# Performance work log

Measured on AMD Instinct MI355X. Metric: run time of the kernel, lower is better.

The kernel has to match this reference:

```python
import jax, jax.numpy as jnp
import numpy as np

B, D, H, W, C = 2, 16, 56, 56, 128
WD, WH, WW = 2, 7, 7
SD, SH, SW = 1, 3, 3
HEADS = 4
HEAD_DIM = C // HEADS
N = WD * WH * WW            # tokens per window = 98
NW = (D // WD) * (H // WH) * (W // WW)  # windows per batch = 512
EPS = 1e-5
SCALE = HEAD_DIM ** -0.5


def _partition_np(x):
    b, d, h, w, c = x.shape
    x = x.reshape(b, d // WD, WD, h // WH, WH, w // WW, WW, c)
    return x.transpose(0, 1, 3, 5, 2, 4, 6, 7).reshape(-1, N, c)


def _compute_attn_mask():
    # cyclic-shift mask: label 3x3x3 regions, windows mix labels -> -100
    img = np.zeros((1, D, H, W, 1), np.float32)
    cnt = 0
    for ds in (slice(0, -WD), slice(-WD, -SD), slice(-SD, None)):
        for hs in (slice(0, -WH), slice(-WH, -SH), slice(-SH, None)):
            for ws in (slice(0, -WW), slice(-WW, -SW), slice(-SW, None)):
                img[:, ds, hs, ws, :] = cnt
                cnt += 1
    mw = _partition_np(img).reshape(-1, N)          # (nW, N)
    am = mw[:, None, :] - mw[:, :, None]
    return np.where(am != 0, -100.0, 0.0).astype(np.float32)


def _rel_index():
    coords = np.stack(np.meshgrid(np.arange(WD), np.arange(WH), np.arange(WW), indexing='ij')).reshape(3, -1)
    rel = (coords[:, :, None] - coords[:, None, :]).transpose(1, 2, 0)  # (N,N,3)
    rel[..., 0] += WD - 1
    rel[..., 1] += WH - 1
    rel[..., 2] += WW - 1
    rel[..., 0] *= (2 * WH - 1) * (2 * WW - 1)
    rel[..., 1] *= 2 * WW - 1
    return rel.sum(-1).astype(np.int32)  # (N,N)


def setup_inputs() -> dict:
    key = jax.random.key(0)
    ks = jax.random.split(key, 8)
    s = 0.02
    table_size = (2 * WD - 1) * (2 * WH - 1) * (2 * WW - 1)
    return {
        'x': jax.random.normal(ks[0], (B, D, H, W, C), jnp.float32),
        'attn_mask': jnp.asarray(_compute_attn_mask()),
        'rel_index': jnp.asarray(_rel_index()),
        'norm1_g': jnp.ones((C,), jnp.float32),
        'norm1_b': jnp.zeros((C,), jnp.float32),
        'qkv_w': jax.random.normal(ks[1], (C, 3 * C), jnp.float32) * s,
        'qkv_b': jnp.zeros((3 * C,), jnp.float32),
        'rel_table': jax.random.normal(ks[2], (table_size, HEADS), jnp.float32) * s,
        'proj_w': jax.random.normal(ks[3], (C, C), jnp.float32) * s,
        'proj_b': jnp.zeros((C,), jnp.float32),
        'norm2_g': jnp.ones((C,), jnp.float32),
        'norm2_b': jnp.zeros((C,), jnp.float32),
        'fc1_w': jax.random.normal(ks[4], (C, 4 * C), jnp.float32) * s,
        'fc1_b': jnp.zeros((4 * C,), jnp.float32),
        'fc2_w': jax.random.normal(ks[5], (4 * C, C), jnp.float32) * s,
        'fc2_b': jnp.zeros((C,), jnp.float32),
    }


def _ln(x, g, b):
    mu = jnp.mean(x, -1, keepdims=True)
    var = jnp.mean(jnp.square(x - mu), -1, keepdims=True)
    return (x - mu) * jax.lax.rsqrt(var + EPS) * g + b


def _block(x, attn_mask, rel_index, norm1_g, norm1_b, qkv_w, qkv_b, rel_table,
           proj_w, proj_b, norm2_g, norm2_b, fc1_w, fc1_b, fc2_w, fc2_b):
    # ---- part1: LN -> shift -> window partition -> W-MSA -> reverse -> unshift
    h = _ln(x, norm1_g, norm1_b)
    h = jnp.roll(h, (-SD, -SH, -SW), axis=(1, 2, 3))
    # window partition -> (B*nW, N, C)
    h = h.reshape(B, D // WD, WD, H // WH, WH, W // WW, WW, C)
    h = h.transpose(0, 1, 3, 5, 2, 4, 6, 7).reshape(B * NW, N, C)
    qkv = (h @ qkv_w + qkv_b).reshape(B * NW, N, 3, HEADS, HEAD_DIM)
    qkv = qkv.transpose(2, 0, 3, 1, 4)  # (3, B_, heads, N, hd)
    q, k, v = qkv[0] * SCALE, qkv[1], qkv[2]
    attn = jnp.einsum('bhnd,bhmd->bhnm', q, k)  # (B_, heads, N, N)
    bias = rel_table[rel_index.reshape(-1)].reshape(N, N, HEADS).transpose(2, 0, 1)
    attn = attn + bias[None]
    attn = attn.reshape(B, NW, HEADS, N, N) + attn_mask[None, :, None]
    attn = jax.nn.softmax(attn.reshape(B * NW, HEADS, N, N), axis=-1)
    o = jnp.einsum('bhnm,bhmd->bhnd', attn, v)
    o = o.transpose(0, 2, 1, 3).reshape(B * NW, N, C)
    o = o @ proj_w + proj_b
    # window reverse -> (B, D, H, W, C)
    o = o.reshape(B, D // WD, H // WH, W // WW, WD, WH, WW, C)
    o = o.transpose(0, 1, 4, 2, 5, 3, 6, 7).reshape(B, D, H, W, C)
    o = jnp.roll(o, (SD, SH, SW), axis=(1, 2, 3))
    x = x + o  # drop_path = identity (rate 0)
    # ---- part2: LN -> MLP (keras gelu is exact, approximate=False)
    m = _ln(x, norm2_g, norm2_b)
    m = jax.nn.gelu(m @ fc1_w + fc1_b, approximate=False) @ fc2_w + fc2_b
    return x + m


def reference(x, attn_mask, rel_index, norm1_g, norm1_b, qkv_w, qkv_b, rel_table,
              proj_w, proj_b, norm2_g, norm2_b, fc1_w, fc1_b, fc2_w, fc2_b):
    return _block(x, attn_mask, rel_index, norm1_g, norm1_b, qkv_w, qkv_b, rel_table,
                  proj_w, proj_b, norm2_g, norm2_b, fc1_w, fc1_b, fc2_w, fc2_b)
```

## Files before the change

### kernel.cpp

```cpp
#include <hip/hip_runtime.h>
#include <math.h>

#define ROWS 100352
#define EPSL 1e-5f
#define SCALE_Q 0.17677669529663687f

typedef __attribute__((ext_vector_type(8))) short bf16x8;
typedef __attribute__((ext_vector_type(4))) float f32x4;

__device__ __forceinline__ unsigned short f2b(float f) {
  union { float f; unsigned int u; } a; a.f = f;
  unsigned int u = a.u;
  return (unsigned short)((u + 0x7FFF + ((u >> 16) & 1)) >> 16);
}

__device__ __forceinline__ int map_row(int r) {
  int t = r;
  int tw = t % 7; t /= 7;
  int th = t % 7; t /= 7;
  int td = t & 1;  t >>= 1;
  int zw = t & 7;  t >>= 3;
  int zh = t & 7;  t >>= 3;
  int zd = t & 7;  int bb = t >> 3;
  int d = zd * 2 + td;
  int h = zh * 7 + th;
  int w = zw * 7 + tw;
  int sd = (d + 1) & 15;
  int sh = h + 3; if (sh >= 56) sh -= 56;
  int sw = w + 3; if (sw >= 56) sw -= 56;
  return ((bb * 16 + sd) * 56 + sh) * 56 + sw;
}

__global__ __launch_bounds__(256) void k_prep_all(
    const float* __restrict__ qkv_w, unsigned short* __restrict__ qkvT,
    const float* __restrict__ proj_w, unsigned short* __restrict__ projT,
    const float* __restrict__ fc1_w, unsigned short* __restrict__ fc1T,
    const float* __restrict__ fc2_w, unsigned short* __restrict__ fc2T)
{
  int b = blockIdx.x, tid = threadIdx.x;
  if (b < 192) {
    int id = b * 256 + tid;
    int n = id >> 7, k = id & 127;
    float v = qkv_w[(size_t)k * 384 + n];
    if (n < 128) v *= SCALE_Q;
    qkvT[id] = f2b(v);
  } else if (b < 256) {
    int id = (b - 192) * 256 + tid;
    int n = id >> 7, k = id & 127;
    projT[id] = f2b(proj_w[(size_t)k * 128 + n]);
  } else if (b < 512) {
    int id = (b - 256) * 256 + tid;
    int n = id >> 7, k = id & 127;
    fc1T[id] = f2b(fc1_w[(size_t)k * 512 + n]);
  } else {
    int id = (b - 512) * 256 + tid;
    int n = id >> 9, k = id & 511;
    fc2T[id] = f2b(fc2_w[(size_t)k * 128 + n]);
  }
}

__global__ __launch_bounds__(256) void k_prep_biasC(
    const int* __restrict__ relidx, const float* __restrict__ rtab,
    float* __restrict__ biasC)
{
  int id = blockIdx.x * 256 + threadIdx.x;
  int l  = id & 63;  int t = id >> 6;
  int ct = t % 7;    t /= 7;
  int rt = t & 7;    t >>= 3;
  int h  = t & 3;    int wm = t >> 2;
  int n0 = rt*16 + ((l >> 4) << 2);
  int m  = ct*16 + (l & 15);
  float4 v;
  float* vp = &v.x;
  int cm = 0;
  if (m < 98)
    cm = (m >= 49 ? 1 : 0) | ((m % 49) >= 28 ? 2 : 0) | ((m % 7) >= 4 ? 4 : 0);
  #pragma unroll
  for (int r = 0; r < 4; ++r) {
    int n = n0 + r;
    float val;
    if (m >= 98) val = -10000.f;
    else if (n >= 98) val = 0.f;
    else {
      val = rtab[relidx[n*98 + m]*4 + h];
      int cn = (n >= 49 ? 1 : 0) | ((n % 49) >= 28 ? 2 : 0) | ((n % 7) >= 4 ? 4 : 0);
      if ((cn ^ cm) & wm) val -= 100.f;
    }
    vp[r] = val;
  }
  *(float4*)(biasC + (size_t)id*4) = v;
}

__global__ __launch_bounds__(256) void k_qkv(
    const float* __restrict__ x, const float* __restrict__ g,
    const float* __restrict__ bta, const unsigned short* __restrict__ Wt,
    const float* __restrict__ bias, unsigned short* __restrict__ out)
{
  __shared__ unsigned short As[128 * 136];
  int tid = threadIdx.x;
  int row0 = blockIdx.x * 128;
  {
    int grp = tid >> 5, lane = tid & 31;
    float4 gv = *(const float4*)(g + lane*4);
    float4 bv = *(const float4*)(bta + lane*4);
    #pragma unroll
    for (int p = 0; p < 16; ++p) {
      int r = p * 8 + grp;
      size_t src = (size_t)map_row(row0 + r);
      float4 v = *(const float4*)(x + src * 128 + lane * 4);
      float s  = v.x + v.y + v.z + v.w;
      float ss = v.x*v.x + v.y*v.y + v.z*v.z + v.w*v.w;
      #pragma unroll
      for (int o = 16; o; o >>= 1) {
        s  += __shfl_xor(s,  o, 32);
        ss += __shfl_xor(ss, o, 32);
      }
      float mu   = s * (1.f/128.f);
      float rstd = rsqrtf(ss * (1.f/128.f) - mu*mu + EPSL);
      ushort4 o4;
      o4.x = f2b((v.x-mu)*rstd*gv.x + bv.x);
      o4.y = f2b((v.y-mu)*rstd*gv.y + bv.y);
      o4.z = f2b((v.z-mu)*rstd*gv.z + bv.z);
      o4.w = f2b((v.w-mu)*rstd*gv.w + bv.w);
      *(ushort4*)&As[r*136 + lane*4] = o4;
    }
  }
  __syncthreads();
  int l = tid & 63, w = tid >> 6;
  int wr = (w >> 1) * 64, wc = (w & 1) * 64;
  int fr = l & 15, gq = l >> 4, fk = gq * 8;
  for (int c = 0; c < 3; ++c) {
    int col0 = c * 128;
    float bmul = (c == 0) ? SCALE_Q : 1.f;
    f32x4 acc[4][4] = {};
    #pragma unroll
    for (int ks = 0; ks < 128; ks += 32) {
      bf16x8 af[4], bv[4];
      #pragma unroll
      for (int n = 0; n < 4; ++n)
        bv[n] = *(const bf16x8*)(Wt + (size_t)(col0 + wc + n*16 + fr)*128 + ks + fk);
      #pragma unroll
      for (int m = 0; m < 4; ++m)
        af[m] = *(bf16x8*)&As[(wr + m*16 + fr)*136 + ks + fk];
      #pragma unroll
      for (int m = 0; m < 4; ++m)
        #pragma unroll
        for (int n = 0; n < 4; ++n)
          acc[m][n] = __builtin_amdgcn_mfma_f32_16x16x32_bf16(af[m], bv[n], acc[m][n], 0, 0, 0);
    }
    #pragma unroll
    for (int m = 0; m < 4; ++m)
      #pragma unroll
      for (int r = 0; r < 4; ++r) {
        int grow = row0 + wr + m*16 + gq*4 + r;
        #pragma unroll
        for (int n = 0; n < 4; ++n) {
          int col = col0 + wc + n*16 + fr;
          out[(size_t)grow*384 + col] = f2b(acc[m][n][r] + bias[col]*bmul);
        }
      }
  }
}

__global__ __launch_bounds__(256, 4) void k_attn_mfma(
    const unsigned short* __restrict__ qkv,
    const float* __restrict__ biasC,
    unsigned short* __restrict__ o_part)
{
  __shared__ unsigned short Vt[32 * 136];
  __shared__ unsigned short Pb[128 * 120];
  int tid  = threadIdx.x;
  int head = blockIdx.x & 3;
  int win  = blockIdx.x >> 2;
  int widx = win & 511;
  int wm = ((widx >> 6) == 7 ? 1 : 0) | (((widx >> 3) & 7) == 7 ? 2 : 0)
         | ((widx & 7) == 7 ? 4 : 0);
  const unsigned short* base = qkv + (size_t)win * 98 * 384 + head * 32;

  for (int it = tid; it < 32 * 128; it += 256) {
    int d = it & 31, m = it >> 5;
    unsigned short v = 0;
    if (m < 98) v = base[m*384 + 256 + d];
    Vt[d*136 + m] = v;
  }
  for (int it = tid; it < 128 * 8; it += 256) {
    int n = it >> 3, c2 = 112 + (it & 7);
    Pb[n*120 + c2] = 0;
  }

  int l = tid & 63, w = tid >> 6;
  int fr = l & 15, g = l >> 4, fk = g * 8;
  bf16x8 zero8 = {0,0,0,0,0,0,0,0};

  bf16x8 aq[2];
  #pragma unroll
  for (int lt = 0; lt < 2; ++lt) {
    int row = (w*2 + lt)*16 + fr;
    aq[lt] = (row < 98) ? *(const bf16x8*)(base + row*384 + fk) : zero8;
  }

  const float* bcb = biasC + (size_t)(wm*4 + head) * 8 * 7 * 256;
  f32x4 S[2][7];
  #pragma unroll
  for (int ct = 0; ct < 7; ++ct) {
    int m = ct*16 + fr;
    bf16x8 kb = (m < 98) ? *(const bf16x8*)(base + m*384 + 128 + fk) : zero8;
    #pragma unroll
    for (int lt = 0; lt < 2; ++lt) {
      f32x4 bc = *(const f32x4*)(bcb + ((w*2 + lt)*7 + ct)*256 + l*4);
      S[lt][ct] = __builtin_amdgcn_mfma_f32_16x16x32_bf16(aq[lt], kb, bc, 0, 0, 0);
    }
  }

  #pragma unroll
  for (int lt = 0; lt < 2; ++lt) {
    #pragma unroll
    for (int r = 0; r < 4; ++r) {
      float mx = S[lt][0][r];
      #pragma unroll
      for (int ct = 1; ct < 7; ++ct) mx = fmaxf(mx, S[lt][ct][r]);
      #pragma unroll
      for (int o = 8; o; o >>= 1) mx = fmaxf(mx, __shfl_xor(mx, o));
      float e[7], sum = 0.f;
      #pragma unroll
      for (int ct = 0; ct < 7; ++ct) { e[ct] = __expf(S[lt][ct][r] - mx); sum += e[ct]; }
      #pragma unroll
      for (int o = 8; o; o >>= 1) sum += __shfl_xor(sum, o);
      float inv = 1.f / sum;
      #pragma unroll
      for (int ct = 0; ct < 7; ++ct) S[lt][ct][r] = e[ct] * inv;
    }
  }

  #pragma unroll
  for (int lt = 0; lt < 2; ++lt)
    #pragma unroll
    for (int ct = 0; ct < 7; ++ct) {
      int m = ct*16 + fr;
      #pragma unroll
      for (int r = 0; r < 4; ++r) {
        int n = w*32 + lt*16 + g*4 + r;
        Pb[n*120 + m] = f2b(S[lt][ct][r]);
      }
    }
  __syncthreads();

  f32x4 O[2][2] = {};
  #pragma unroll
  for (int ks = 0; ks < 4; ++ks) {
    bf16x8 ap[2], bv[2];
    #pragma unroll
    for (int lt = 0; lt < 2; ++lt) {
      int rowoff = ((w*2 + lt)*16 + fr)*120;
      if (ks < 3) ap[lt] = *(bf16x8*)&Pb[rowoff + ks*32 + fk];
      else        ap[lt] = (g < 2) ? *(bf16x8*)&Pb[rowoff + 96 + fk] : zero8;
    }
    #pragma unroll
    for (int vt = 0; vt < 2; ++vt)
      bv[vt] = *(bf16x8*)&Vt[(vt*16 + fr)*136 + ks*32 + fk];
    #pragma unroll
    for (int lt = 0; lt < 2; ++lt)
      #pragma unroll
      for (int vt = 0; vt < 2; ++vt)
        O[lt][vt] = __builtin_amdgcn_mfma_f32_16x16x32_bf16(ap[lt], bv[vt], O[lt][vt], 0, 0, 0);
  }

  #pragma unroll
  for (int lt = 0; lt < 2; ++lt)
    #pragma unroll
    for (int r = 0; r < 4; ++r) {
      int n = w*32 + lt*16 + g*4 + r;
      if (n < 98) {
        unsigned short* orow = o_part + ((size_t)win*98 + n)*128 + head*32;
        #pragma unroll
        for (int vt = 0; vt < 2; ++vt)
          orow[vt*16 + fr] = f2b(O[lt][vt][r]);
      }
    }
}

__global__ __launch_bounds__(256) void k_proj(
    const unsigned short* __restrict__ A,
    const unsigned short* __restrict__ Wt,
    const float* __restrict__ bias,
    const float* __restrict__ Xres, float* __restrict__ Cf)
{
  __shared__ unsigned short As[128 * 136];
  int tid = threadIdx.x;
  int row0 = blockIdx.x * 128;
  #pragma unroll
  for (int i = 0; i < 8; ++i) {
    int chunk = i * 256 + tid;
    int rr = chunk >> 4, off = (chunk & 15) * 8;
    *(uint4*)&As[rr*136 + off] = *(const uint4*)(A + (size_t)(row0+rr)*128 + off);
  }
  __syncthreads();
  int l = tid & 63, w = tid >> 6;
  int wr = (w >> 1) * 64, wc = (w & 1) * 64;
  int fr = l & 15, gq = l >> 4, fk = gq * 8;
  f32x4 acc[4][4] = {};
  #pragma unroll
  for (int ks = 0; ks < 128; ks += 32) {
    bf16x8 af[4], bv[4];
    #pragma unroll
    for (int n = 0; n < 4; ++n)
      bv[n] = *(const bf16x8*)(Wt + (size_t)(wc + n*16 + fr)*128 + ks + fk);
    #pragma unroll
    for (int m = 0; m < 4; ++m)
      af[m] = *(bf16x8*)&As[(wr + m*16 + fr)*136 + ks + fk];
    #pragma unroll
    for (int m = 0; m < 4; ++m)
      #pragma unroll
      for (int n = 0; n < 4; ++n)
        acc[m][n] = __builtin_amdgcn_mfma_f32_16x16x32_bf16(af[m], bv[n], acc[m][n], 0, 0, 0);
  }
  #pragma unroll
  for (int m = 0; m < 4; ++m)
    #pragma unroll
    for (int r = 0; r < 4; ++r) {
      int grow = row0 + wr + m*16 + gq*4 + r;
      size_t dst = (size_t)map_row(grow);
      #pragma unroll
      for (int n = 0; n < 4; ++n) {
        int col = wc + n*16 + fr;
        Cf[dst*128 + col] = acc[m][n][r] + bias[col] + Xres[dst*128 + col];
      }
    }
}

__global__ __launch_bounds__(512, 4) void k_mlp(
    float* __restrict__ xio,
    const float* __restrict__ g, const float* __restrict__ bta,
    const unsigned short* __restrict__ W1t,
    const float* __restrict__ b1,
    const unsigned short* __restrict__ W2t,
    const float* __restrict__ b2)
{
  __shared__ unsigned short As[128 * 136];
  __shared__ unsigned short Pb[128 * 136];
  int tid = threadIdx.x;
  int row0 = blockIdx.x * 128;
  {
    int grp = tid >> 5, lane = tid & 31;
    float4 gv = *(const float4*)(g + lane*4);
    float4 bv = *(const float4*)(bta + lane*4);
    #pragma unroll
    for (int p = 0; p < 8; ++p) {
      int r = p * 16 + grp;
      float4 v = *(const float4*)(xio + (size_t)(row0 + r) * 128 + lane * 4);
      float s  = v.x + v.y + v.z + v.w;
      float ss = v.x*v.x + v.y*v.y + v.z*v.z + v.w*v.w;
      #pragma unroll
      for (int o = 16; o; o >>= 1) {
        s  += __shfl_xor(s,  o, 32);
        ss += __shfl_xor(ss, o, 32);
      }
      float mu   = s * (1.f/128.f);
      float rstd = rsqrtf(ss * (1.f/128.f) - mu*mu + EPSL);
      ushort4 o4;
      o4.x = f2b((v.x-mu)*rstd*gv.x + bv.x);
      o4.y = f2b((v.y-mu)*rstd*gv.y + bv.y);
      o4.z = f2b((v.z-mu)*rstd*gv.z + bv.z);
      o4.w = f2b((v.w-mu)*rstd*gv.w + bv.w);
      *(ushort4*)&As[r*136 + lane*4] = o4;
    }
  }
  __syncthreads();
  int l = tid & 63, w = tid >> 6;
  int wr = (w & 1) * 64, wc = (w >> 1) * 32;
  int fr = l & 15, gq = l >> 4, fk = gq * 8;

  f32x4 O[4][2] = {};
  for (int j = 0; j < 4; ++j) {
    f32x4 S[4][2] = {};
    #pragma unroll
    for (int ks = 0; ks < 4; ++ks) {
      bf16x8 af[4], bv[2];
      #pragma unroll
      for (int n = 0; n < 2; ++n)
        bv[n] = *(const bf16x8*)(W1t + (size_t)(j*128 + wc + n*16 + fr)*128 + ks*32 + fk);
      #pragma unroll
      for (int m = 0; m < 4; ++m)
        af[m] = *(bf16x8*)&As[(wr + m*16 + fr)*136 + ks*32 + fk];
      #pragma unroll
      for (int m = 0; m < 4; ++m)
        #pragma unroll
        for (int n = 0; n < 2; ++n)
          S[m][n] = __builtin_amdgcn_mfma_f32_16x16x32_bf16(af[m], bv[n], S[m][n], 0, 0, 0);
    }
    #pragma unroll
    for (int m = 0; m < 4; ++m)
      #pragma unroll
      for (int n = 0; n < 2; ++n) {
        int col = wc + n*16 + fr;
        float bb = b1[j*128 + col];
        #pragma unroll
        for (int r = 0; r < 4; ++r) {
          float v = S[m][n][r] + bb;
          float u = 1.5957691216057308f * v * (1.f + 0.044715f*v*v);
          v = v / (1.f + __expf(-u));
          Pb[(wr + m*16 + gq*4 + r)*136 + col] = f2b(v);
        }
      }
    __syncthreads();
    #pragma unroll
    for (int ks = 0; ks < 4; ++ks) {
      bf16x8 ap[4], bv[2];
      #pragma unroll
      for (int n = 0; n < 2; ++n)
        bv[n] = *(const bf16x8*)(W2t + (size_t)(wc + n*16 + fr)*512 + j*128 + ks*32 + fk);
      #pragma unroll
      for (int m = 0; m < 4; ++m)
        ap[m] = *(bf16x8*)&Pb[(wr + m*16 + fr)*136 + ks*32 + fk];
      #pragma unroll
      for (int m = 0; m < 4; ++m)
        #pragma unroll
        for (int n = 0; n < 2; ++n)
          O[m][n] = __builtin_amdgcn_mfma_f32_16x16x32_bf16(ap[m], bv[n], O[m][n], 0, 0, 0);
    }
    __syncthreads();
  }
  #pragma unroll
  for (int m = 0; m < 4; ++m)
    #pragma unroll
    for (int r = 0; r < 4; ++r) {
      size_t grow = row0 + wr + m*16 + gq*4 + r;
      #pragma unroll
      for (int n = 0; n < 2; ++n) {
        int col = wc + n*16 + fr;
        xio[grow*128 + col] += O[m][n][r] + b2[col];
      }
    }
}

extern "C" void kernel_launch(void* const* d_in, const int* in_sizes, int n_in,
                              void* d_out, int out_size, void* d_ws, size_t ws_size,
                              hipStream_t stream)
{
  const float* x         = (const float*)d_in[0];
  const int*   rel_index = (const int*)  d_in[2];
  const float* n1g       = (const float*)d_in[3];
  const float* n1b       = (const float*)d_in[4];
  const float* qkv_w     = (const float*)d_in[5];
  const float* qkv_b     = (const float*)d_in[6];
  const float* rtab      = (const float*)d_in[7];
  const float* proj_w    = (const float*)d_in[8];
  const float* proj_b    = (const float*)d_in[9];
  const float* n2g       = (const float*)d_in[10];
  const float* n2b       = (const float*)d_in[11];
  const float* fc1_w     = (const float*)d_in[12];
  const float* fc1_b     = (const float*)d_in[13];
  const float* fc2_w     = (const float*)d_in[14];
  const float* fc2_b     = (const float*)d_in[15];
  float* out = (float*)d_out;

  unsigned short* buf0  = (unsigned short*)d_ws;
  unsigned short* buf1  = buf0 + (size_t)ROWS * 384;
  unsigned short* qkvT  = buf1 + (size_t)ROWS * 128;
  unsigned short* projT = qkvT + 384 * 128;
  unsigned short* fc1T  = projT + 128 * 128;
  unsigned short* fc2T  = fc1T + 512 * 128;
  float* biasC          = (float*)(fc2T + 128 * 512);

  k_prep_all<<<768, 256, 0, stream>>>(qkv_w, qkvT, proj_w, projT,
                                      fc1_w, fc1T, fc2_w, fc2T);
  k_prep_biasC<<<448, 256, 0, stream>>>(rel_index, rtab, biasC);

  k_qkv<<<ROWS/128, 256, 0, stream>>>(x, n1g, n1b, qkvT, qkv_b, buf0);

  k_attn_mfma<<<4096, 256, 0, stream>>>(buf0, biasC, buf1);

  k_proj<<<ROWS/128, 256, 0, stream>>>(buf1, projT, proj_b, x, out);

  k_mlp<<<ROWS/128, 512, 0, stream>>>(out, n2g, n2b, fc1T, fc1_b, fc2T, fc2_b);
}
```

Before: 238.1 us.

## Register-resident MLP: fold LN affine into fc1, drop LDS staging via bpermute

Rewrites the MLP kernel so each wave owns 32 tokens, keeps the normalized activations and the GELU hidden tile in registers, and uses the swapped-operand MFMA layout with ds_bpermute to reshape the hidden fragments instead of staging through shared memory with block barriers. The LayerNorm gamma is folded into the fc1 weights, and beta into a precomputed fc1 bias by a new small prep kernel. This removes LDS traffic and __syncthreads from the hot loop. In exchange each wave re-reads the weights from global/L2, register pressure rises (O[8][2] accumulators), and bf16 packing now uses the hardware cvt instruction.

```diff
diff --git a/kernel.cpp b/kernel.cpp
--- a/kernel.cpp
+++ b/kernel.cpp
@@ -12,6 +12,11 @@
   union { float f; unsigned int u; } a; a.f = f;
   unsigned int u = a.u;
   return (unsigned short)((u + 0x7FFF + ((u >> 16) & 1)) >> 16);
+}
+__device__ __forceinline__ unsigned cvtpk(float lo, float hi) {
+  unsigned r;
+  asm volatile("v_cvt_pk_bf16_f32 %0, %1, %2" : "=v"(r) : "v"(lo), "v"(hi));
+  return r;
 }
 
 __device__ __forceinline__ int map_row(int r) {
@@ -35,7 +40,8 @@
     const float* __restrict__ qkv_w, unsigned short* __restrict__ qkvT,
     const float* __restrict__ proj_w, unsigned short* __restrict__ projT,
     const float* __restrict__ fc1_w, unsigned short* __restrict__ fc1T,
-    const float* __restrict__ fc2_w, unsigned short* __restrict__ fc2T)
+    const float* __restrict__ fc2_w, unsigned short* __restrict__ fc2T,
+    const float* __restrict__ n2g)
 {
   int b = blockIdx.x, tid = threadIdx.x;
   if (b < 192) {
@@ -51,12 +57,23 @@
   } else if (b < 512) {
     int id = (b - 256) * 256 + tid;
     int n = id >> 7, k = id & 127;
-    fc1T[id] = f2b(fc1_w[(size_t)k * 512 + n]);
+    fc1T[id] = f2b(fc1_w[(size_t)k * 512 + n] * n2g[k]);
   } else {
     int id = (b - 512) * 256 + tid;
     int n = id >> 9, k = id & 511;
     fc2T[id] = f2b(fc2_w[(size_t)k * 128 + n]);
   }
+}
+
+__global__ __launch_bounds__(256) void k_prep_b1(
+    const float* __restrict__ fc1_b, const float* __restrict__ n2b,
+    const float* __restrict__ fc1_w, float* __restrict__ b1p)
+{
+  int h = blockIdx.x * 256 + threadIdx.x;
+  if (h >= 512) return;
+  float acc = fc1_b[h];
+  for (int k = 0; k < 128; ++k) acc += n2b[k] * fc1_w[(size_t)k * 512 + h];
+  b1p[h] = acc;
 }
 
 __global__ __launch_bounds__(256) void k_prep_biasC(
@@ -328,109 +345,132 @@
     }
 }
 
-__global__ __launch_bounds__(512, 4) void k_mlp(
+__global__ __launch_bounds__(256, 3) void k_mlp(
     float* __restrict__ xio,
-    const float* __restrict__ g, const float* __restrict__ bta,
     const unsigned short* __restrict__ W1t,
-    const float* __restrict__ b1,
+    const float* __restrict__ b1p,
     const unsigned short* __restrict__ W2t,
     const float* __restrict__ b2)
 {
-  __shared__ unsigned short As[128 * 136];
-  __shared__ unsigned short Pb[128 * 136];
   int tid = threadIdx.x;
-  int row0 = blockIdx.x * 128;
-  {
-    int grp = tid >> 5, lane = tid & 31;
-    float4 gv = *(const float4*)(g + lane*4);
-    float4 bv = *(const float4*)(bta + lane*4);
-    #pragma unroll
-    for (int p = 0; p < 8; ++p) {
-      int r = p * 16 + grp;
-      float4 v = *(const float4*)(xio + (size_t)(row0 + r) * 128 + lane * 4);
-      float s  = v.x + v.y + v.z + v.w;
-      float ss = v.x*v.x + v.y*v.y + v.z*v.z + v.w*v.w;
-      #pragma unroll
-      for (int o = 16; o; o >>= 1) {
-        s  += __shfl_xor(s,  o, 32);
-        ss += __shfl_xor(ss, o, 32);
-      }
-      float mu   = s * (1.f/128.f);
-      float rstd = rsqrtf(ss * (1.f/128.f) - mu*mu + EPSL);
-      ushort4 o4;
-      o4.x = f2b((v.x-mu)*rstd*gv.x + bv.x);
-      o4.y = f2b((v.y-mu)*rstd*gv.y + bv.y);
-      o4.z = f2b((v.z-mu)*rstd*gv.z + bv.z);
-      o4.w = f2b((v.w-mu)*rstd*gv.w + bv.w);
-      *(ushort4*)&As[r*136 + lane*4] = o4;
-    }
-  }
-  __syncthreads();
   int l = tid & 63, w = tid >> 6;
-  int wr = (w & 1) * 64, wc = (w >> 1) * 32;
-  int fr = l & 15, gq = l >> 4, fk = gq * 8;
-
-  f32x4 O[4][2] = {};
-  for (int j = 0; j < 4; ++j) {
-    f32x4 S[4][2] = {};
+  int i = l & 15, gl = l >> 4;
+  int fk = gl * 8;
+  int tok0 = blockIdx.x * 128 + w * 32;
+
+  int idx0 = (((l >> 4) & 1) * 32 + i) * 4;
+  int idx1 = idx0 + 64;
+  bool hiHalf = (l >= 32);
+
+  bf16x8 atok[2][4];
+  #pragma unroll
+  for (int t = 0; t < 2; ++t) {
+    const float* row = xio + (size_t)(tok0 + t*16 + i) * 128;
+    float v[4][8];
+    float s = 0.f, ss = 0.f;
     #pragma unroll
     for (int ks = 0; ks < 4; ++ks) {
-      bf16x8 af[4], bv[2];
-      #pragma unroll
-      for (int n = 0; n < 2; ++n)
-        bv[n] = *(const bf16x8*)(W1t + (size_t)(j*128 + wc + n*16 + fr)*128 + ks*32 + fk);
-      #pragma unroll
-      for (int m = 0; m < 4; ++m)
-        af[m] = *(bf16x8*)&As[(wr + m*16 + fr)*136 + ks*32 + fk];
-      #pragma unroll
-      for (int m = 0; m < 4; ++m)
+      float4 v0 = *(const float4*)(row + ks*32 + fk);
+      float4 v1 = *(const float4*)(row + ks*32 + fk + 4);
+      v[ks][0]=v0.x; v[ks][1]=v0.y; v[ks][2]=v0.z; v[ks][3]=v0.w;
+      v[ks][4]=v1.x; v[ks][5]=v1.y; v[ks][6]=v1.z; v[ks][7]=v1.w;
+      s += v0.x+v0.y+v0.z+v0.w + v1.x+v1.y+v1.z+v1.w;
+      ss += v0.x*v0.x+v0.y*v0.y+v0.z*v0.z+v0.w*v0.w
+          + v1.x*v1.x+v1.y*v1.y+v1.z*v1.z+v1.w*v1.w;
+    }
+    s  += __shfl_xor(s, 16);  s  += __shfl_xor(s, 32);
+    ss += __shfl_xor(ss, 16); ss += __shfl_xor(ss, 32);
+    float mu = s * (1.f/128.f);
+    float rstd = rsqrtf(ss * (1.f/128.f) - mu*mu + EPSL);
+    #pragma unroll
+    for (int ks = 0; ks < 4; ++ks) {
+      union { unsigned u[4]; bf16x8 v8; } pk;
+      #pragma unroll
+      for (int p = 0; p < 4; ++p)
+        pk.u[p] = cvtpk((v[ks][2*p]-mu)*rstd, (v[ks][2*p+1]-mu)*rstd);
+      atok[t][ks] = pk.v8;
+    }
+  }
+
+  f32x4 O[8][2] = {};
+  for (int j = 0; j < 16; ++j) {
+    f32x4 S[2][2] = {{{0.f,0.f,0.f,0.f},{0.f,0.f,0.f,0.f}},
+                     {{0.f,0.f,0.f,0.f},{0.f,0.f,0.f,0.f}}};
+    #pragma unroll
+    for (int ks = 0; ks < 4; ++ks) {
+      bf16x8 w1f[2];
+      #pragma unroll
+      for (int T = 0; T < 2; ++T)
+        w1f[T] = *(const bf16x8*)(W1t + (size_t)(j*32 + T*16 + i)*128 + ks*32 + fk);
+      #pragma unroll
+      for (int T = 0; T < 2; ++T)
         #pragma unroll
-        for (int n = 0; n < 2; ++n)
-          S[m][n] = __builtin_amdgcn_mfma_f32_16x16x32_bf16(af[m], bv[n], S[m][n], 0, 0, 0);
-    }
-    #pragma unroll
-    for (int m = 0; m < 4; ++m)
-      #pragma unroll
-      for (int n = 0; n < 2; ++n) {
-        int col = wc + n*16 + fr;
-        float bb = b1[j*128 + col];
+        for (int t = 0; t < 2; ++t)
+          S[T][t] = __builtin_amdgcn_mfma_f32_16x16x32_bf16(w1f[T], atok[t][ks], S[T][t], 0, 0, 0);
+    }
+    float b1v[2][4];
+    #pragma unroll
+    for (int T = 0; T < 2; ++T)
+      #pragma unroll
+      for (int r = 0; r < 4; ++r)
+        b1v[T][r] = b1p[j*32 + T*16 + gl*4 + r];
+    #pragma unroll
+    for (int T = 0; T < 2; ++T)
+      #pragma unroll
+      for (int t = 0; t < 2; ++t)
         #pragma unroll
         for (int r = 0; r < 4; ++r) {
-          float v = S[m][n][r] + bb;
-          float u = 1.5957691216057308f * v * (1.f + 0.044715f*v*v);
-          v = v / (1.f + __expf(-u));
-          Pb[(wr + m*16 + gq*4 + r)*136 + col] = f2b(v);
+          float vv = S[T][t][r] + b1v[T][r];
+          float u = 1.5957691216057308f * vv * (1.f + 0.044715f*vv*vv);
+          S[T][t][r] = vv / (1.f + __expf(-u));
         }
-      }
-    __syncthreads();
-    #pragma unroll
-    for (int ks = 0; ks < 4; ++ks) {
-      bf16x8 ap[4], bv[2];
-      #pragma unroll
-      for (int n = 0; n < 2; ++n)
-        bv[n] = *(const bf16x8*)(W2t + (size_t)(wc + n*16 + fr)*512 + j*128 + ks*32 + fk);
-      #pragma unroll
-      for (int m = 0; m < 4; ++m)
-        ap[m] = *(bf16x8*)&Pb[(wr + m*16 + fr)*136 + ks*32 + fk];
-      #pragma unroll
-      for (int m = 0; m < 4; ++m)
-        #pragma unroll
-        for (int n = 0; n < 2; ++n)
-          O[m][n] = __builtin_amdgcn_mfma_f32_16x16x32_bf16(ap[m], bv[n], O[m][n], 0, 0, 0);
-    }
-    __syncthreads();
-  }
-  #pragma unroll
-  for (int m = 0; m < 4; ++m)
-    #pragma unroll
-    for (int r = 0; r < 4; ++r) {
-      size_t grow = row0 + wr + m*16 + gq*4 + r;
-      #pragma unroll
-      for (int n = 0; n < 2; ++n) {
-        int col = wc + n*16 + fr;
-        xio[grow*128 + col] += O[m][n][r] + b2[col];
-      }
-    }
+    bf16x8 pf[2];
+    #pragma unroll
+    for (int t = 0; t < 2; ++t) {
+      int A = (int)cvtpk(S[0][t][0], S[0][t][1]);
+      int B = (int)cvtpk(S[0][t][2], S[0][t][3]);
+      int C = (int)cvtpk(S[1][t][0], S[1][t][1]);
+      int D = (int)cvtpk(S[1][t][2], S[1][t][3]);
+      union { unsigned u[4]; bf16x8 v8; } pk;
+      int a0 = __builtin_amdgcn_ds_bpermute(idx0, A);
+      int c0 = __builtin_amdgcn_ds_bpermute(idx0, C);
+      int b0 = __builtin_amdgcn_ds_bpermute(idx0, B);
+      int d0 = __builtin_amdgcn_ds_bpermute(idx0, D);
+      int a1 = __builtin_amdgcn_ds_bpermute(idx1, A);
+      int c1 = __builtin_amdgcn_ds_bpermute(idx1, C);
+      int b1r = __builtin_amdgcn_ds_bpermute(idx1, B);
+      int d1 = __builtin_amdgcn_ds_bpermute(idx1, D);
+      pk.u[0] = (unsigned)(hiHalf ? c0 : a0);
+      pk.u[1] = (unsigned)(hiHalf ? d0 : b0);
+      pk.u[2] = (unsigned)(hiHalf ? c1 : a1);
+      pk.u[3] = (unsigned)(hiHalf ? d1 : b1r);
+      pf[t] = pk.v8;
+    }
+    #pragma unroll
+    for (int jt = 0; jt < 8; ++jt) {
+      bf16x8 w2f = *(const bf16x8*)(W2t + (size_t)(jt*16 + i)*512 + j*32 + fk);
+      #pragma unroll
+      for (int t = 0; t < 2; ++t)
+        O[jt][t] = __builtin_amdgcn_mfma_f32_16x16x32_bf16(w2f, pf[t], O[jt][t], 0, 0, 0);
+    }
+  }
+
+  #pragma unroll
+  for (int t = 0; t < 2; ++t) {
+    float* row = xio + (size_t)(tok0 + t*16 + i) * 128;
+    #pragma unroll
+    for (int jt = 0; jt < 8; ++jt) {
+      int col = jt*16 + gl*4;
+      float4 res = *(const float4*)(row + col);
+      float4 bv = *(const float4*)(b2 + col);
+      float4 o4;
+      o4.x = res.x + O[jt][t][0] + bv.x;
+      o4.y = res.y + O[jt][t][1] + bv.y;
+      o4.z = res.z + O[jt][t][2] + bv.z;
+      o4.w = res.w + O[jt][t][3] + bv.w;
+      *(float4*)(row + col) = o4;
+    }
+  }
 }
 
 extern "C" void kernel_launch(void* const* d_in, const int* in_sizes, int n_in,
@@ -461,10 +501,12 @@
   unsigned short* fc1T  = projT + 128 * 128;
   unsigned short* fc2T  = fc1T + 512 * 128;
   float* biasC          = (float*)(fc2T + 128 * 512);
+  float* b1p            = biasC + 458752;
 
   k_prep_all<<<768, 256, 0, stream>>>(qkv_w, qkvT, proj_w, projT,
-                                      fc1_w, fc1T, fc2_w, fc2T);
+                                      fc1_w, fc1T, fc2_w, fc2T, n2g);
   k_prep_biasC<<<448, 256, 0, stream>>>(rel_index, rtab, biasC);
+  k_prep_b1<<<2, 256, 0, stream>>>(fc1_b, n2b, fc1_w, b1p);
 
   k_qkv<<<ROWS/128, 256, 0, stream>>>(x, n1g, n1b, qkvT, qkv_b, buf0);
 
@@ -472,5 +514,5 @@
 
   k_proj<<<ROWS/128, 256, 0, stream>>>(buf1, projT, proj_b, x, out);
 
-  k_mlp<<<ROWS/128, 512, 0, stream>>>(out, n2g, n2b, fc1T, fc1_b, fc2T, fc2_b);
-}
+  k_mlp<<<ROWS/128, 256, 0, stream>>>(out, fc1T, b1p, fc2T, fc2_b);
+}
```

Measured after the change: 314.2 us. +31.9%, slower.

## Split LN2 into its own kernel, fold gamma/beta into fc1, remap attention block order

Applied to the files above, without the earlier changes.

Moves the second LayerNorm out of the MLP kernel into a separate kernel that writes normalized bf16 rows to a workspace buffer. The LN affine parameters are folded into fc1 weights and a precomputed bias, so the MLP kernel just copies bf16 rows into shared memory. The attention grid is also remapped so consecutive blocks are spread across windows in strides of 512. This adds an extra launch and an extra round trip of a bf16 activation tensor through memory, in exchange for a lighter MLP prologue.

```diff
diff --git a/kernel.cpp b/kernel.cpp
--- a/kernel.cpp
+++ b/kernel.cpp
@@ -35,7 +35,8 @@
     const float* __restrict__ qkv_w, unsigned short* __restrict__ qkvT,
     const float* __restrict__ proj_w, unsigned short* __restrict__ projT,
     const float* __restrict__ fc1_w, unsigned short* __restrict__ fc1T,
-    const float* __restrict__ fc2_w, unsigned short* __restrict__ fc2T)
+    const float* __restrict__ fc2_w, unsigned short* __restrict__ fc2T,
+    const float* __restrict__ n2g)
 {
   int b = blockIdx.x, tid = threadIdx.x;
   if (b < 192) {
@@ -51,12 +52,23 @@
   } else if (b < 512) {
     int id = (b - 256) * 256 + tid;
     int n = id >> 7, k = id & 127;
-    fc1T[id] = f2b(fc1_w[(size_t)k * 512 + n]);
+    fc1T[id] = f2b(fc1_w[(size_t)k * 512 + n] * n2g[k]);
   } else {
     int id = (b - 512) * 256 + tid;
     int n = id >> 9, k = id & 511;
     fc2T[id] = f2b(fc2_w[(size_t)k * 128 + n]);
   }
+}
+
+__global__ __launch_bounds__(256) void k_prep_b1(
+    const float* __restrict__ fc1_b, const float* __restrict__ n2b,
+    const float* __restrict__ fc1_w, float* __restrict__ b1p)
+{
+  int h = blockIdx.x * 256 + threadIdx.x;
+  if (h >= 512) return;
+  float acc = fc1_b[h];
+  for (int k = 0; k < 128; ++k) acc += n2b[k] * fc1_w[(size_t)k * 512 + h];
+  b1p[h] = acc;
 }
 
 __global__ __launch_bounds__(256) void k_prep_biasC(
@@ -170,8 +182,10 @@
   __shared__ unsigned short Vt[32 * 136];
   __shared__ unsigned short Pb[128 * 120];
   int tid  = threadIdx.x;
-  int head = blockIdx.x & 3;
-  int win  = blockIdx.x >> 2;
+  int bid  = blockIdx.x;
+  int wg   = (bid & 7) * 512 + (bid >> 3);
+  int head = wg & 3;
+  int win  = wg >> 2;
   int widx = win & 511;
   int wm = ((widx >> 6) == 7 ? 1 : 0) | (((widx >> 3) & 7) == 7 ? 2 : 0)
          | ((widx & 7) == 7 ? 4 : 0);
@@ -328,11 +342,35 @@
     }
 }
 
+__global__ __launch_bounds__(256) void k_ln2(
+    const float* __restrict__ x, unsigned short* __restrict__ out)
+{
+  int tid = threadIdx.x;
+  int grp = tid >> 5, lane = tid & 31;
+  size_t r = (size_t)blockIdx.x * 8 + grp;
+  float4 v = *(const float4*)(x + r * 128 + lane * 4);
+  float s  = v.x + v.y + v.z + v.w;
+  float ss = v.x*v.x + v.y*v.y + v.z*v.z + v.w*v.w;
+  #pragma unroll
+  for (int o = 16; o; o >>= 1) {
+    s  += __shfl_xor(s,  o, 32);
+    ss += __shfl_xor(ss, o, 32);
+  }
+  float mu   = s * (1.f/128.f);
+  float rstd = rsqrtf(ss * (1.f/128.f) - mu*mu + EPSL);
+  ushort4 o4;
+  o4.x = f2b((v.x-mu)*rstd);
+  o4.y = f2b((v.y-mu)*rstd);
+  o4.z = f2b((v.z-mu)*rstd);
+  o4.w = f2b((v.w-mu)*rstd);
+  *(ushort4*)(out + r*128 + lane*4) = o4;
+}
+
 __global__ __launch_bounds__(512, 4) void k_mlp(
     float* __restrict__ xio,
-    const float* __restrict__ g, const float* __restrict__ bta,
+    const unsigned short* __restrict__ h2,
     const unsigned short* __restrict__ W1t,
-    const float* __restrict__ b1,
+    const float* __restrict__ b1p,
     const unsigned short* __restrict__ W2t,
     const float* __restrict__ b2)
 {
@@ -340,30 +378,11 @@
   __shared__ unsigned short Pb[128 * 136];
   int tid = threadIdx.x;
   int row0 = blockIdx.x * 128;
-  {
-    int grp = tid >> 5, lane = tid & 31;
-    float4 gv = *(const float4*)(g + lane*4);
-    float4 bv = *(const float4*)(bta + lane*4);
-    #pragma unroll
-    for (int p = 0; p < 8; ++p) {
-      int r = p * 16 + grp;
-      float4 v = *(const float4*)(xio + (size_t)(row0 + r) * 128 + lane * 4);
-      float s  = v.x + v.y + v.z + v.w;
-      float ss = v.x*v.x + v.y*v.y + v.z*v.z + v.w*v.w;
-      #pragma unroll
-      for (int o = 16; o; o >>= 1) {
-        s  += __shfl_xor(s,  o, 32);
-        ss += __shfl_xor(ss, o, 32);
-      }
-      float mu   = s * (1.f/128.f);
-      float rstd = rsqrtf(ss * (1.f/128.f) - mu*mu + EPSL);
-      ushort4 o4;
-      o4.x = f2b((v.x-mu)*rstd*gv.x + bv.x);
-      o4.y = f2b((v.y-mu)*rstd*gv.y + bv.y);
-      o4.z = f2b((v.z-mu)*rstd*gv.z + bv.z);
-      o4.w = f2b((v.w-mu)*rstd*gv.w + bv.w);
-      *(ushort4*)&As[r*136 + lane*4] = o4;
-    }
+  #pragma unroll
+  for (int i = 0; i < 4; ++i) {
+    int chunk = i * 512 + tid;
+    int rr = chunk >> 4, off = (chunk & 15) * 8;
+    *(uint4*)&As[rr*136 + off] = *(const uint4*)(h2 + (size_t)(row0+rr)*128 + off);
   }
   __syncthreads();
   int l = tid & 63, w = tid >> 6;
@@ -393,7 +412,7 @@
       #pragma unroll
       for (int n = 0; n < 2; ++n) {
         int col = wc + n*16 + fr;
-        float bb = b1[j*128 + col];
+        float bb = b1p[j*128 + col];
         #pragma unroll
         for (int r = 0; r < 4; ++r) {
           float v = S[m][n][r] + bb;
@@ -461,10 +480,12 @@
   unsigned short* fc1T  = projT + 128 * 128;
   unsigned short* fc2T  = fc1T + 512 * 128;
   float* biasC          = (float*)(fc2T + 128 * 512);
+  float* b1p            = biasC + 458752;
 
   k_prep_all<<<768, 256, 0, stream>>>(qkv_w, qkvT, proj_w, projT,
-                                      fc1_w, fc1T, fc2_w, fc2T);
+                                      fc1_w, fc1T, fc2_w, fc2T, n2g);
   k_prep_biasC<<<448, 256, 0, stream>>>(rel_index, rtab, biasC);
+  k_prep_b1<<<2, 256, 0, stream>>>(fc1_b, n2b, fc1_w, b1p);
 
   k_qkv<<<ROWS/128, 256, 0, stream>>>(x, n1g, n1b, qkvT, qkv_b, buf0);
 
@@ -472,5 +493,7 @@
 
   k_proj<<<ROWS/128, 256, 0, stream>>>(buf1, projT, proj_b, x, out);
 
-  k_mlp<<<ROWS/128, 512, 0, stream>>>(out, n2g, n2b, fc1T, fc1_b, fc2T, fc2_b);
-}
+  k_ln2<<<ROWS/8, 256, 0, stream>>>(out, buf0);
+
+  k_mlp<<<ROWS/128, 512, 0, stream>>>(out, buf0, fc1T, b1p, fc2T, fc2_b);
+}
```

New measurement: 247.0 us. 3.7% more time.
